# Kernel tuning notes

Hardware: AMD Instinct MI355X
Metric: run time of the kernel (lower is better)

Reference implementation:

```python
import jax, jax.numpy as jnp
import numpy as np


def setup_inputs() -> dict:
    key = jax.random.key(0)
    k1, k2, k3 = jax.random.split(key, 3)
    bs, nvars, T, input_dim = 8, 16, 512, 256
    embed_dim, num_embed, codebook_num = 128, 512, 4
    inp = jax.random.normal(k1, (bs, nvars, T, input_dim), dtype=jnp.float32)
    # xavier_normal_ for (input_dim, embed_dim): std = sqrt(2/(fan_in+fan_out))
    xavier_std = float(np.sqrt(2.0 / (input_dim + embed_dim)))
    projector = jax.random.normal(k2, (input_dim, embed_dim), dtype=jnp.float32) * xavier_std
    codebook = jax.random.normal(k3, (codebook_num, num_embed, embed_dim), dtype=jnp.float32)
    return {"input": inp, "projector": projector, "codebook": codebook}


def reference(input, projector, codebook):
    # project: [b,n,t,input_dim] @ [input_dim,embed_dim] -> [b,n,t,d]
    x = jnp.matmul(input, projector)
    # L2-normalize along last dim (matches torch .norm(dim=-1,keepdim=True) division)
    x = x / jnp.linalg.norm(x, axis=-1, keepdims=True)
    cb = codebook / jnp.linalg.norm(codebook, axis=-1, keepdims=True)
    # cosine similarity: [b,n,t,c,m]
    similarity = jnp.einsum('bntd,cmd->bntcm', x, cb)
    # nearest code per codebook: [b,n,t,c]
    idx = jnp.argmax(similarity, axis=-1)
    return idx
```

## Files before the change

### kernel.cpp

```cpp
#include <hip/hip_runtime.h>
#include <math.h>

#define DIN    256
#define DEMB   128
#define NCB    4
#define MCODES 512
#define NCODE  2048
#define MARGIN 1.5e-4f

using bf16x8 = __attribute__((ext_vector_type(8))) short;
using f32x16 = __attribute__((ext_vector_type(16))) float;

static __device__ __forceinline__ unsigned short f2bf(float f) {
    unsigned u = __float_as_uint(f);
    u += 0x7FFFu + ((u >> 16) & 1u);
    return (unsigned short)(u >> 16);
}
static __device__ __forceinline__ float bf2f(unsigned short h) {
    return __uint_as_float(((unsigned)h) << 16);
}
static __device__ __forceinline__ float4 ld4(const float* p) {
    return *reinterpret_cast<const float4*>(p);
}
static __device__ __forceinline__ void gload_lds16(const void* g, void* l) {
    __builtin_amdgcn_global_load_lds(
        (const __attribute__((address_space(1))) void*)g,
        (__attribute__((address_space(3))) void*)l, 16, 0, 0);
}

__global__ __launch_bounds__(256) void prep_codebook(
        const float* __restrict__ cb, float* __restrict__ cbn,
        unsigned short* __restrict__ cbA) {
    const int w = threadIdx.x >> 6, lane = threadIdx.x & 63;
    const int code = blockIdx.x * 4 + w;
    const float2 v = reinterpret_cast<const float2*>(cb + (size_t)code * DEMB)[lane];
    float ss = v.x * v.x + v.y * v.y;
#pragma unroll
    for (int m = 1; m < 64; m <<= 1) ss += __shfl_xor(ss, m, 64);
    const float rn = 1.0f / sqrtf(ss);
    const float x0 = v.x * rn, x1 = v.y * rn;
    reinterpret_cast<float2*>(cbn + (size_t)code * DEMB)[lane] = make_float2(x0, x1);

    const unsigned short h0 = f2bf(x0), h1 = f2bf(x1);
    const unsigned short l0 = f2bf(x0 - bf2f(h0)), l1 = f2bf(x1 - bf2f(h1));
    const int ct = code >> 5, ci = code & 31;
    const int kt = lane >> 3, g = (lane >> 2) & 1, i = 2 * (lane & 3);
    const size_t base = ((size_t)ct * 1024 + kt * 128 + g * 32 + ci) * 8 + i;
    *reinterpret_cast<ushort2*>(cbA + base)       = make_ushort2(h0, h1);
    *reinterpret_cast<ushort2*>(cbA + base + 512) = make_ushort2(l0, l1);
}

__global__ __launch_bounds__(256) void prep_proj(
        const float* __restrict__ proj, unsigned short* __restrict__ pjA) {
    const int t = blockIdx.x * 256 + threadIdx.x;
    const int ci = t & 31, g = (t >> 5) & 1, kt = (t >> 6) & 15, mt = t >> 10;
    const int m = mt * 32 + ci;
    const size_t base = ((size_t)(mt * 16 + kt) * 3) * 512 + (size_t)(g * 32 + ci) * 8;
#pragma unroll
    for (int i = 0; i < 8; ++i) {
        const float v = proj[(size_t)(kt * 16 + g * 8 + i) * DEMB + m];
        const unsigned short h = f2bf(v);
        const float r1 = v - bf2f(h);
        const unsigned short md = f2bf(r1);
        const float r2 = r1 - bf2f(md);
        pjA[base + i]        = h;
        pjA[base + 512 + i]  = md;
        pjA[base + 1024 + i] = f2bf(r2);
    }
}

__global__ __launch_bounds__(256) void project_mfma(
        const float* __restrict__ inp, const unsigned short* __restrict__ pjA,
        float* __restrict__ xw) {
    const int tid = threadIdx.x;
    const int lane = tid & 63, mt = tid >> 6, kg = lane >> 5;
    const int row = blockIdx.x * 32 + (lane & 31);
    const float* xr = inp + (size_t)row * DIN;
    const unsigned short* pL = pjA + (size_t)lane * 8;

    auto ldin = [&](float4& a, float4& b, int kt) {
        a = ld4(xr + kt * 16 + kg * 8);
        b = ld4(xr + kt * 16 + kg * 8 + 4);
    };

    f32x16 P, Q;
#pragma unroll
    for (int r = 0; r < 16; ++r) { P[r] = 0.0f; Q[r] = 0.0f; }

    auto do_step = [&](const float4& c0, const float4& c1, int kt) {
        const float xs[8] = {c0.x, c0.y, c0.z, c0.w, c1.x, c1.y, c1.z, c1.w};
        bf16x8 Bh, Bm, Bl;
#pragma unroll
        for (int e = 0; e < 8; ++e) {
            const float v = xs[e];
            const unsigned short h = f2bf(v);
            const float r1 = v - bf2f(h);
            const unsigned short md = f2bf(r1);
            const float r2 = r1 - bf2f(md);
            Bh[e] = (short)h; Bm[e] = (short)md; Bl[e] = (short)f2bf(r2);
        }
        const unsigned short* pf = pL + ((size_t)(mt * 16 + kt) * 3) * 512;
        const bf16x8 Ah = *reinterpret_cast<const bf16x8*>(pf);
        const bf16x8 Am = *reinterpret_cast<const bf16x8*>(pf + 512);
        const bf16x8 Al = *reinterpret_cast<const bf16x8*>(pf + 1024);
        P = __builtin_amdgcn_mfma_f32_32x32x16_bf16(Ah, Bh, P, 0, 0, 0);
        Q = __builtin_amdgcn_mfma_f32_32x32x16_bf16(Ah, Bm, Q, 0, 0, 0);
        Q = __builtin_amdgcn_mfma_f32_32x32x16_bf16(Am, Bh, Q, 0, 0, 0);
        Q = __builtin_amdgcn_mfma_f32_32x32x16_bf16(Ah, Bl, Q, 0, 0, 0);
        Q = __builtin_amdgcn_mfma_f32_32x32x16_bf16(Al, Bh, Q, 0, 0, 0);
        Q = __builtin_amdgcn_mfma_f32_32x32x16_bf16(Am, Bm, Q, 0, 0, 0);
    };

    float4 nA0, nA1, nB0, nB1;
    ldin(nA0, nA1, 0);
#pragma unroll 1
    for (int kt = 0; kt < 16; kt += 2) {
        ldin(nB0, nB1, kt + 1);
        do_step(nA0, nA1, kt);
        if (kt + 2 < 16) ldin(nA0, nA1, kt + 2);
        do_step(nB0, nB1, kt + 1);
    }

#pragma unroll
    for (int q = 0; q < 4; ++q) {
        float4 v;
        v.x = P[q * 4 + 0] + Q[q * 4 + 0];
        v.y = P[q * 4 + 1] + Q[q * 4 + 1];
        v.z = P[q * 4 + 2] + Q[q * 4 + 2];
        v.w = P[q * 4 + 3] + Q[q * 4 + 3];
        *reinterpret_cast<float4*>(xw + (size_t)row * DEMB + mt * 32 + q * 8 + kg * 4) = v;
    }
}

__global__ __launch_bounds__(256) void project_kernel(
        const float* __restrict__ inp, const float* __restrict__ proj,
        float* __restrict__ xw) {
    const int tid = threadIdx.x, tx = tid & 31, ty = tid >> 5;
    const int rowBase = blockIdx.x * 64;

    float acc1[8][4];
#pragma unroll
    for (int i = 0; i < 8; ++i)
#pragma unroll
        for (int j = 0; j < 4; ++j) acc1[i][j] = 0.0f;

    const float* inRow0 = inp + (size_t)(rowBase + ty) * DIN;
    const float* pjCol  = proj + tx * 4;

    float4 ivA[8], ivB[8], pjA[4], pjB[4];
    auto load_step = [&](float4 iv[8], float4 pj[4], int kk) {
#pragma unroll
        for (int j = 0; j < 4; ++j) pj[j] = ld4(pjCol + (size_t)(kk + j) * DEMB);
#pragma unroll
        for (int i = 0; i < 8; ++i) iv[i] = ld4(inRow0 + (size_t)(8 * i) * DIN + kk);
    };
    auto fma_step = [&](const float4 iv[8], const float4 pj[4]) {
#pragma unroll
        for (int i = 0; i < 8; ++i) {
            const float* ivp = reinterpret_cast<const float*>(&iv[i]);
#pragma unroll
            for (int j = 0; j < 4; ++j) {
                acc1[i][0] = fmaf(ivp[j], pj[j].x, acc1[i][0]);
                acc1[i][1] = fmaf(ivp[j], pj[j].y, acc1[i][1]);
                acc1[i][2] = fmaf(ivp[j], pj[j].z, acc1[i][2]);
                acc1[i][3] = fmaf(ivp[j], pj[j].w, acc1[i][3]);
            }
        }
    };
    load_step(ivA, pjA, 0);
#pragma unroll 1
    for (int k = 0; k < DIN; k += 8) {
        load_step(ivB, pjB, k + 4);
        fma_step(ivA, pjA);
        if (k + 8 < DIN) load_step(ivA, pjA, k + 8);
        fma_step(ivB, pjB);
    }
#pragma unroll
    for (int i = 0; i < 8; ++i) {
        const int r = rowBase + ty + 8 * i;
        *reinterpret_cast<float4*>(xw + (size_t)r * DEMB + tx * 4) =
            make_float4(acc1[i][0], acc1[i][1], acc1[i][2], acc1[i][3]);
    }
}

__global__ __launch_bounds__(256) void sim_kernel(
        const float* __restrict__ xw,
        const unsigned short* __restrict__ cbA,
        int* __restrict__ out, int* __restrict__ unc_cnt,
        int* __restrict__ unc_list) {
    __shared__ __align__(16) short sA[3][8192];
    const int tid = threadIdx.x;
    const int lane = tid & 63, wv = tid >> 6;
    const int kg = lane >> 5;
    const int cbi = blockIdx.x & 3;
    const int rowBase = (blockIdx.x >> 2) * 128;
    const int row = rowBase + wv * 32 + (lane & 31);

    const short* gA = (const short*)cbA + (size_t)cbi * 16 * 8192;
    auto stage = [&](int buf, int t) {
        const short* g = gA + (size_t)t * 8192 + wv * 2048 + lane * 8;
        short* l = &sA[buf][wv * 2048];
#pragma unroll
        for (int c = 0; c < 4; ++c)
            gload_lds16(g + c * 512, l + c * 512);
    };

    stage(0, 0);
    stage(1, 1);

    bf16x8 Bhi[8], Blo[8];
    {
        const float* xr = xw + (size_t)row * DEMB;
        float4 f0[8], f1[8];
        float ss = 0.0f;
#pragma unroll
        for (int kt = 0; kt < 8; ++kt) {
            f0[kt] = ld4(xr + kt * 16 + kg * 8);
            f1[kt] = ld4(xr + kt * 16 + kg * 8 + 4);
            ss += f0[kt].x * f0[kt].x + f0[kt].y * f0[kt].y +
                  f0[kt].z * f0[kt].z + f0[kt].w * f0[kt].w +
                  f1[kt].x * f1[kt].x + f1[kt].y * f1[kt].y +
                  f1[kt].z * f1[kt].z + f1[kt].w * f1[kt].w;
        }
        ss += __shfl_xor(ss, 32, 64);
        const float rn = 1.0f / sqrtf(ss);
#pragma unroll
        for (int kt = 0; kt < 8; ++kt) {
            const float xs[8] = {f0[kt].x, f0[kt].y, f0[kt].z, f0[kt].w,
                                 f1[kt].x, f1[kt].y, f1[kt].z, f1[kt].w};
            bf16x8 hv, lv;
#pragma unroll
            for (int e = 0; e < 8; ++e) {
                const float xn = xs[e] * rn;
                const unsigned short h = f2bf(xn);
                hv[e] = (short)h;
                lv[e] = (short)f2bf(xn - bf2f(h));
            }
            Bhi[kt] = hv; Blo[kt] = lv;
        }
    }

    f32x16 TWO;
#pragma unroll
    for (int r = 0; r < 16; ++r) TWO[r] = 2.0f;

    f32x16 acc = TWO;
    float t1 = -INFINITY, t2 = -INFINITY; int i1 = 0;

#pragma unroll 1
    for (int g = 0; g < 16; ++g) {
        if (g < 15) asm volatile("s_waitcnt vmcnt(4)" ::: "memory");
        else        asm volatile("s_waitcnt vmcnt(0)" ::: "memory");
        __builtin_amdgcn_s_barrier();
        asm volatile("" ::: "memory");
        if (g + 2 < 16) stage((g + 2) % 3, g + 2);

        const short* pa = &sA[g % 3][lane * 8];
        const f32x16 pAcc = acc;
        __builtin_amdgcn_s_setprio(1);
#pragma unroll
        for (int kt = 0; kt < 8; ++kt) {
            const bf16x8 Ahi = *reinterpret_cast<const bf16x8*>(pa + kt * 1024);
            const bf16x8 Alo = *reinterpret_cast<const bf16x8*>(pa + kt * 1024 + 512);
            acc = __builtin_amdgcn_mfma_f32_32x32x16_bf16(Ahi, Bhi[kt], kt ? acc : TWO, 0, 0, 0);
            acc = __builtin_amdgcn_mfma_f32_32x32x16_bf16(Ahi, Blo[kt], acc, 0, 0, 0);
            acc = __builtin_amdgcn_mfma_f32_32x32x16_bf16(Alo, Bhi[kt], acc, 0, 0, 0);
        }
        __builtin_amdgcn_s_setprio(0);

        if (g > 0) {
            const int base = (g - 1) * 32;
#pragma unroll
            for (int r = 0; r < 16; ++r) {
                const float v = pAcc[r];
                const int gidx = base + (r & 3) + 8 * (r >> 2) + 4 * kg;
                t2 = fmaxf(t2, fminf(v, t1));
                if (v > t1) { t1 = v; i1 = gidx; }
            }
        }
    }
    {
        const int base = 15 * 32;
#pragma unroll
        for (int r = 0; r < 16; ++r) {
            const float v = acc[r];
            const int gidx = base + (r & 3) + 8 * (r >> 2) + 4 * kg;
            t2 = fmaxf(t2, fminf(v, t1));
            if (v > t1) { t1 = v; i1 = gidx; }
        }
    }

    const float o1 = __shfl_xor(t1, 32, 64);
    const float o2 = __shfl_xor(t2, 32, 64);
    const int   oi = __shfl_xor(i1, 32, 64);
    const float m2 = fmaxf(fmaxf(t2, o2), fminf(t1, o1));
    if (o1 > t1 || (o1 == t1 && oi < i1)) { t1 = o1; i1 = oi; }
    const bool unc = (t1 - m2) < MARGIN;
    if (lane < 32 && !unc)
        out[(size_t)row * NCB + cbi] = i1;

    unsigned long long msk = __ballot(unc && lane < 32);
    if (lane == 0 && msk) {
        const int n = __popcll(msk);
        int base = atomicAdd(unc_cnt, n);
        while (msk) {
            const int r = __ffsll(msk) - 1; msk &= msk - 1;
            unc_list[base++] = ((rowBase + wv * 32 + r) << 2) | cbi;
        }
    }
}

__global__ __launch_bounds__(256) void recheck_kernel(
        const float* __restrict__ inp, const float* __restrict__ proj,
        const float* __restrict__ cbn,
        const int* __restrict__ unc_cnt, const int* __restrict__ unc_list,
        int* __restrict__ out) {
    __shared__ float sx[4][DEMB];
    const int lane = threadIdx.x & 63, wv = threadIdx.x >> 6;
    const int n = *unc_cnt;
    for (int it = blockIdx.x * 4 + wv; it < n; it += gridDim.x * 4) {
        const int item = unc_list[it];
        const int row = item >> 2, cbi = item & 3;
        {
            const float* ir = inp + (size_t)row * DIN;
            float a0 = 0.0f, a1 = 0.0f;
#pragma unroll 2
            for (int k = 0; k < DIN; k += 4) {
                const float4 iv = ld4(ir + k);
                const float* ivp = reinterpret_cast<const float*>(&iv);
#pragma unroll
                for (int j = 0; j < 4; ++j) {
                    a0 = fmaf(ivp[j], proj[(size_t)(k + j) * DEMB + lane],      a0);
                    a1 = fmaf(ivp[j], proj[(size_t)(k + j) * DEMB + lane + 64], a1);
                }
            }
            sx[wv][lane] = a0; sx[wv][lane + 64] = a1;
        }
        float best = -INFINITY; int bi = 0;
#pragma unroll 2
        for (int j = 0; j < 8; ++j) {
            const int c = lane + 64 * j;
            const float* cv = cbn + ((size_t)cbi * MCODES + c) * DEMB;
            float s0 = 0, s1 = 0, s2 = 0, s3 = 0;
#pragma unroll 4
            for (int k = 0; k < DEMB; k += 4) {
                const float4 xk = ld4(&sx[wv][k]);
                const float4 ck = ld4(cv + k);
                s0 = fmaf(xk.x, ck.x, s0); s1 = fmaf(xk.y, ck.y, s1);
                s2 = fmaf(xk.z, ck.z, s2); s3 = fmaf(xk.w, ck.w, s3);
            }
            const float s = (s0 + s1) + (s2 + s3);
            if (s > best) { best = s; bi = c; }
        }
#pragma unroll
        for (int mm = 1; mm < 64; mm <<= 1) {
            const float ov = __shfl_xor(best, mm, 64);
            const int   oc = __shfl_xor(bi, mm, 64);
            if (ov > best || (ov == best && oc < bi)) { best = ov; bi = oc; }
        }
        if (lane == 0) out[(size_t)row * NCB + cbi] = bi;
    }
}

__global__ __launch_bounds__(256) void fused_quantize_kernel(
        const float* __restrict__ inp, const float* __restrict__ proj,
        const float* __restrict__ cbn, const unsigned short* __restrict__ cbA,
        int* __restrict__ out) {
    __shared__ float sX[128][132];
    __shared__ float sRn[128];
    const int tid = threadIdx.x;
    const int tx = tid & 31, ty = tid >> 5;
    const int rowBase = blockIdx.x * 128;

#pragma unroll 1
    for (int p = 0; p < 2; ++p) {
        float acc1[8][4];
#pragma unroll
        for (int i = 0; i < 8; ++i)
#pragma unroll
            for (int j = 0; j < 4; ++j) acc1[i][j] = 0.0f;
        const float* inRow0 = inp + (size_t)(rowBase + p * 64 + ty) * DIN;
        const float* pjCol  = proj + tx * 4;
        float4 ivA[8], ivB[8], pjA[4], pjB[4];
        auto load_step = [&](float4 iv[8], float4 pj[4], int kk) {
#pragma unroll
            for (int j = 0; j < 4; ++j) pj[j] = ld4(pjCol + (size_t)(kk + j) * DEMB);
#pragma unroll
            for (int i = 0; i < 8; ++i) iv[i] = ld4(inRow0 + (size_t)(8 * i) * DIN + kk);
        };
        auto fma_step = [&](const float4 iv[8], const float4 pj[4]) {
#pragma unroll
            for (int i = 0; i < 8; ++i) {
                const float* ivp = reinterpret_cast<const float*>(&iv[i]);
#pragma unroll
                for (int j = 0; j < 4; ++j) {
                    acc1[i][0] = fmaf(ivp[j], pj[j].x, acc1[i][0]);
                    acc1[i][1] = fmaf(ivp[j], pj[j].y, acc1[i][1]);
                    acc1[i][2] = fmaf(ivp[j], pj[j].z, acc1[i][2]);
                    acc1[i][3] = fmaf(ivp[j], pj[j].w, acc1[i][3]);
                }
            }
        };
        load_step(ivA, pjA, 0);
#pragma unroll 1
        for (int k = 0; k < DIN; k += 8) {
            load_step(ivB, pjB, k + 4);
            fma_step(ivA, pjA);
            if (k + 8 < DIN) load_step(ivA, pjA, k + 8);
            fma_step(ivB, pjB);
        }
#pragma unroll
        for (int i = 0; i < 8; ++i) {
            const int r = p * 64 + ty + 8 * i;
            float ss = acc1[i][0] * acc1[i][0] + acc1[i][1] * acc1[i][1] +
                       acc1[i][2] * acc1[i][2] + acc1[i][3] * acc1[i][3];
#pragma unroll
            for (int mm = 1; mm < 32; mm <<= 1) ss += __shfl_xor(ss, mm, 64);
            if (tx == 0) sRn[r] = 1.0f / sqrtf(ss);
            *reinterpret_cast<float4*>(&sX[r][tx * 4]) =
                make_float4(acc1[i][0], acc1[i][1], acc1[i][2], acc1[i][3]);
        }
    }
    __syncthreads();

    const int lane = tid & 63, wv = tid >> 6;
    const int kg = lane >> 5;
    const int rowL = wv * 32 + (lane & 31);
    bf16x8 Bhi[8], Blo[8];
    {
        const float rn = sRn[rowL];
#pragma unroll
        for (int kt = 0; kt < 8; ++kt) {
            const int k0 = kt * 16 + kg * 8;
            float4 f0 = ld4(&sX[rowL][k0]);
            float4 f1 = ld4(&sX[rowL][k0 + 4]);
            float xs[8] = {f0.x, f0.y, f0.z, f0.w, f1.x, f1.y, f1.z, f1.w};
            bf16x8 hv, lv;
#pragma unroll
            for (int e = 0; e < 8; ++e) {
                const float xn = xs[e] * rn;
                const unsigned short h = f2bf(xn);
                hv[e] = (short)h;
                lv[e] = (short)f2bf(xn - bf2f(h));
            }
            Bhi[kt] = hv; Blo[kt] = lv;
        }
    }
    float t1 = -INFINITY, t2 = -INFINITY; int i1 = 0;
    const short* pA = reinterpret_cast<const short*>(cbA) + (size_t)lane * 8;
#pragma unroll 1
    for (int ct = 0; ct < 64; ++ct) {
        if ((ct & 1) == 0) __syncthreads();
        const short* pct = pA + (size_t)ct * 8192;
        f32x16 accA, accB;
#pragma unroll
        for (int r = 0; r < 16; ++r) { accA[r] = 0.0f; accB[r] = 0.0f; }
#pragma unroll
        for (int kt = 0; kt < 8; ++kt) {
            const bf16x8 Ahi = *reinterpret_cast<const bf16x8*>(pct + kt * 1024);
            const bf16x8 Alo = *reinterpret_cast<const bf16x8*>(pct + kt * 1024 + 512);
            accA = __builtin_amdgcn_mfma_f32_32x32x16_bf16(Ahi, Bhi[kt], accA, 0, 0, 0);
            accB = __builtin_amdgcn_mfma_f32_32x32x16_bf16(Ahi, Blo[kt], accB, 0, 0, 0);
            accB = __builtin_amdgcn_mfma_f32_32x32x16_bf16(Alo, Bhi[kt], accB, 0, 0, 0);
        }
#pragma unroll
        for (int r = 0; r < 16; ++r) {
            const float v = accA[r] + accB[r];
            const int gidx = ct * 32 + ((r & 3) + 8 * (r >> 2) + 4 * kg);
            t2 = fmaxf(t2, fminf(v, t1));
            if (v > t1) { t1 = v; i1 = gidx; }
        }
        if ((ct & 15) == 15) {
            const int cbi = ct >> 4;
            const float o1 = __shfl_xor(t1, 32, 64);
            const float o2 = __shfl_xor(t2, 32, 64);
            const int   oi = __shfl_xor(i1, 32, 64);
            const float m2 = fmaxf(fmaxf(t2, o2), fminf(t1, o1));
            if (o1 > t1 || (o1 == t1 && oi < i1)) { t1 = o1; i1 = oi; }
            const bool unc = (t1 - m2) < MARGIN;
            if (lane < 32 && !unc)
                out[(size_t)(rowBase + rowL) * NCB + cbi] = i1 - cbi * MCODES;
            unsigned long long msk = __ballot(unc && lane < 32);
            while (msk) {
                const int r = __ffsll(msk) - 1; msk &= msk - 1;
                const int rl = wv * 32 + r;
                float best = -INFINITY; int bi = 0;
#pragma unroll 1
                for (int j = 0; j < 8; ++j) {
                    const int c = lane + 64 * j;
                    const float* cv = cbn + ((size_t)cbi * MCODES + c) * DEMB;
                    float s0 = 0, s1 = 0, s2 = 0, s3 = 0;
#pragma unroll
                    for (int k = 0; k < DEMB; k += 4) {
                        const float4 xk = ld4(&sX[rl][k]);
                        const float4 ck = ld4(cv + k);
                        s0 = fmaf(xk.x, ck.x, s0); s1 = fmaf(xk.y, ck.y, s1);
                        s2 = fmaf(xk.z, ck.z, s2); s3 = fmaf(xk.w, ck.w, s3);
                    }
                    const float s = (s0 + s1) + (s2 + s3);
                    if (s > best) { best = s; bi = c; }
                }
#pragma unroll
                for (int mm = 1; mm < 64; mm <<= 1) {
                    const float ov = __shfl_xor(best, mm, 64);
                    const int   oc = __shfl_xor(bi, mm, 64);
                    if (ov > best || (ov == best && oc < bi)) { best = ov; bi = oc; }
                }
                if (lane == 0) out[(size_t)(rowBase + rl) * NCB + cbi] = bi;
            }
            t1 = -INFINITY; t2 = -INFINITY; i1 = 0;
        }
    }
}

extern "C" void kernel_launch(void* const* d_in, const int* in_sizes, int n_in,
                              void* d_out, int out_size, void* d_ws, size_t ws_size,
                              hipStream_t stream) {
    const float* inp  = (const float*)d_in[0];
    const float* proj = (const float*)d_in[1];
    const float* cb   = (const float*)d_in[2];
    int* out = (int*)d_out;

    char* ws = (char*)d_ws;
    float* cbn = (float*)ws;
    unsigned short* cbA = (unsigned short*)(ws + (1 << 20));
    float* xw  = (float*)(ws + (2 << 20) + (1 << 18));
    const size_t off_cnt = (size_t)(2 << 20) + (1 << 18) + ((size_t)32 << 20);
    int* unc_cnt  = (int*)(ws + off_cnt);
    int* unc_list = (int*)(ws + off_cnt + 256);
    const size_t off_pjA = off_cnt + 256 + (1 << 20);
    unsigned short* pjA = (unsigned short*)(ws + off_pjA);
    const size_t need_old = off_pjA;
    const size_t need_new = off_pjA + 192 * 1024;

    hipLaunchKernelGGL(prep_codebook, dim3(NCODE / 4), dim3(256), 0, stream,
                       cb, cbn, cbA);
    if (ws_size >= need_old) {
        hipMemsetAsync(unc_cnt, 0, 4, stream);
        if (ws_size >= need_new) {
            hipLaunchKernelGGL(prep_proj, dim3(16), dim3(256), 0, stream, proj, pjA);
            hipLaunchKernelGGL(project_mfma, dim3(2048), dim3(256), 0, stream,
                               inp, pjA, xw);
        } else {
            hipLaunchKernelGGL(project_kernel, dim3(1024), dim3(256), 0, stream,
                               inp, proj, xw);
        }
        hipLaunchKernelGGL(sim_kernel, dim3(2048), dim3(256), 0, stream,
                           xw, cbA, out, unc_cnt, unc_list);
        hipLaunchKernelGGL(recheck_kernel, dim3(1024), dim3(256), 0, stream,
                           inp, proj, cbn, unc_cnt, unc_list, out);
    } else {
        hipLaunchKernelGGL(fused_quantize_kernel, dim3(512), dim3(256), 0, stream,
                           inp, proj, cbn, cbA, out);
    }
}
```

Measured before the change: 234.8 us.

## Load codebook fragments directly from global into registers, drop LDS staging

```diff
diff --git a/kernel.cpp b/kernel.cpp
--- a/kernel.cpp
+++ b/kernel.cpp
@@ -21,11 +21,6 @@
 }
 static __device__ __forceinline__ float4 ld4(const float* p) {
     return *reinterpret_cast<const float4*>(p);
-}
-static __device__ __forceinline__ void gload_lds16(const void* g, void* l) {
-    __builtin_amdgcn_global_load_lds(
-        (const __attribute__((address_space(1))) void*)g,
-        (__attribute__((address_space(3))) void*)l, 16, 0, 0);
 }
 
 __global__ __launch_bounds__(256) void prep_codebook(
@@ -82,12 +77,19 @@
         a = ld4(xr + kt * 16 + kg * 8);
         b = ld4(xr + kt * 16 + kg * 8 + 4);
     };
+    auto ldA = [&](bf16x8& h, bf16x8& m, bf16x8& l, int kt) {
+        const unsigned short* pf = pL + ((size_t)(mt * 16 + kt) * 3) * 512;
+        h = *reinterpret_cast<const bf16x8*>(pf);
+        m = *reinterpret_cast<const bf16x8*>(pf + 512);
+        l = *reinterpret_cast<const bf16x8*>(pf + 1024);
+    };
 
     f32x16 P, Q;
 #pragma unroll
     for (int r = 0; r < 16; ++r) { P[r] = 0.0f; Q[r] = 0.0f; }
 
-    auto do_step = [&](const float4& c0, const float4& c1, int kt) {
+    auto do_step = [&](const float4& c0, const float4& c1,
+                       const bf16x8& Ah, const bf16x8& Am, const bf16x8& Al) {
         const float xs[8] = {c0.x, c0.y, c0.z, c0.w, c1.x, c1.y, c1.z, c1.w};
         bf16x8 Bh, Bm, Bl;
 #pragma unroll
@@ -99,10 +101,6 @@
             const float r2 = r1 - bf2f(md);
             Bh[e] = (short)h; Bm[e] = (short)md; Bl[e] = (short)f2bf(r2);
         }
-        const unsigned short* pf = pL + ((size_t)(mt * 16 + kt) * 3) * 512;
-        const bf16x8 Ah = *reinterpret_cast<const bf16x8*>(pf);
-        const bf16x8 Am = *reinterpret_cast<const bf16x8*>(pf + 512);
-        const bf16x8 Al = *reinterpret_cast<const bf16x8*>(pf + 1024);
         P = __builtin_amdgcn_mfma_f32_32x32x16_bf16(Ah, Bh, P, 0, 0, 0);
         Q = __builtin_amdgcn_mfma_f32_32x32x16_bf16(Ah, Bm, Q, 0, 0, 0);
         Q = __builtin_amdgcn_mfma_f32_32x32x16_bf16(Am, Bh, Q, 0, 0, 0);
@@ -111,14 +109,17 @@
         Q = __builtin_amdgcn_mfma_f32_32x32x16_bf16(Am, Bm, Q, 0, 0, 0);
     };
 
-    float4 nA0, nA1, nB0, nB1;
-    ldin(nA0, nA1, 0);
+    float4 iA0, iA1, iB0, iB1;
+    bf16x8 hA, mA, lA, hB, mB, lB;
+    ldin(iA0, iA1, 0); ldA(hA, mA, lA, 0);
+    ldin(iB0, iB1, 1); ldA(hB, mB, lB, 1);
+
 #pragma unroll 1
     for (int kt = 0; kt < 16; kt += 2) {
-        ldin(nB0, nB1, kt + 1);
-        do_step(nA0, nA1, kt);
-        if (kt + 2 < 16) ldin(nA0, nA1, kt + 2);
-        do_step(nB0, nB1, kt + 1);
+        do_step(iA0, iA1, hA, mA, lA);
+        if (kt + 2 < 16) { ldin(iA0, iA1, kt + 2); ldA(hA, mA, lA, kt + 2); }
+        do_step(iB0, iB1, hB, mB, lB);
+        if (kt + 3 < 16) { ldin(iB0, iB1, kt + 3); ldA(hB, mB, lB, kt + 3); }
     }
 
 #pragma unroll
@@ -188,25 +189,12 @@
         const unsigned short* __restrict__ cbA,
         int* __restrict__ out, int* __restrict__ unc_cnt,
         int* __restrict__ unc_list) {
-    __shared__ __align__(16) short sA[3][8192];
     const int tid = threadIdx.x;
     const int lane = tid & 63, wv = tid >> 6;
     const int kg = lane >> 5;
     const int cbi = blockIdx.x & 3;
     const int rowBase = (blockIdx.x >> 2) * 128;
     const int row = rowBase + wv * 32 + (lane & 31);
-
-    const short* gA = (const short*)cbA + (size_t)cbi * 16 * 8192;
-    auto stage = [&](int buf, int t) {
-        const short* g = gA + (size_t)t * 8192 + wv * 2048 + lane * 8;
-        short* l = &sA[buf][wv * 2048];
-#pragma unroll
-        for (int c = 0; c < 4; ++c)
-            gload_lds16(g + c * 512, l + c * 512);
-    };
-
-    stage(0, 0);
-    stage(1, 1);
 
     bf16x8 Bhi[8], Blo[8];
     {
@@ -240,47 +228,42 @@
         }
     }
 
+    const short* gA = (const short*)cbA + (size_t)cbi * 16 * 8192 + lane * 8;
+    bf16x8 Ah0, Al0, Ah1, Al1;
+    auto lda = [&](bf16x8& h, bf16x8& l, int s) {
+        const short* p = gA + (size_t)s * 1024;
+        h = *reinterpret_cast<const bf16x8*>(p);
+        l = *reinterpret_cast<const bf16x8*>(p + 512);
+    };
+    lda(Ah0, Al0, 0);
+    lda(Ah1, Al1, 1);
+
     f32x16 TWO;
 #pragma unroll
     for (int r = 0; r < 16; ++r) TWO[r] = 2.0f;
 
-    f32x16 acc = TWO;
     float t1 = -INFINITY, t2 = -INFINITY; int i1 = 0;
 
 #pragma unroll 1
     for (int g = 0; g < 16; ++g) {
-        if (g < 15) asm volatile("s_waitcnt vmcnt(4)" ::: "memory");
-        else        asm volatile("s_waitcnt vmcnt(0)" ::: "memory");
-        __builtin_amdgcn_s_barrier();
-        asm volatile("" ::: "memory");
-        if (g + 2 < 16) stage((g + 2) % 3, g + 2);
-
-        const short* pa = &sA[g % 3][lane * 8];
-        const f32x16 pAcc = acc;
-        __builtin_amdgcn_s_setprio(1);
+        f32x16 acc;
+        const int s0 = g * 8;
 #pragma unroll
         for (int kt = 0; kt < 8; ++kt) {
-            const bf16x8 Ahi = *reinterpret_cast<const bf16x8*>(pa + kt * 1024);
-            const bf16x8 Alo = *reinterpret_cast<const bf16x8*>(pa + kt * 1024 + 512);
-            acc = __builtin_amdgcn_mfma_f32_32x32x16_bf16(Ahi, Bhi[kt], kt ? acc : TWO, 0, 0, 0);
-            acc = __builtin_amdgcn_mfma_f32_32x32x16_bf16(Ahi, Blo[kt], acc, 0, 0, 0);
-            acc = __builtin_amdgcn_mfma_f32_32x32x16_bf16(Alo, Bhi[kt], acc, 0, 0, 0);
-        }
-        __builtin_amdgcn_s_setprio(0);
-
-        if (g > 0) {
-            const int base = (g - 1) * 32;
-#pragma unroll
-            for (int r = 0; r < 16; ++r) {
-                const float v = pAcc[r];
-                const int gidx = base + (r & 3) + 8 * (r >> 2) + 4 * kg;
-                t2 = fmaxf(t2, fminf(v, t1));
-                if (v > t1) { t1 = v; i1 = gidx; }
-            }
-        }
-    }
-    {
-        const int base = 15 * 32;
+            const int nx = (s0 + kt + 2 < 128) ? s0 + kt + 2 : 127;
+            if ((kt & 1) == 0) {
+                acc = __builtin_amdgcn_mfma_f32_32x32x16_bf16(Ah0, Bhi[kt], kt ? acc : TWO, 0, 0, 0);
+                acc = __builtin_amdgcn_mfma_f32_32x32x16_bf16(Ah0, Blo[kt], acc, 0, 0, 0);
+                acc = __builtin_amdgcn_mfma_f32_32x32x16_bf16(Al0, Bhi[kt], acc, 0, 0, 0);
+                lda(Ah0, Al0, nx);
+            } else {
+                acc = __builtin_amdgcn_mfma_f32_32x32x16_bf16(Ah1, Bhi[kt], acc, 0, 0, 0);
+                acc = __builtin_amdgcn_mfma_f32_32x32x16_bf16(Ah1, Blo[kt], acc, 0, 0, 0);
+                acc = __builtin_amdgcn_mfma_f32_32x32x16_bf16(Al1, Bhi[kt], acc, 0, 0, 0);
+                lda(Ah1, Al1, nx);
+            }
+        }
+        const int base = g * 32;
 #pragma unroll
         for (int r = 0; r < 16; ++r) {
             const float v = acc[r];
```

Result: slower. 275.9 us (+17.5%).
